# Optimization experiments

Measured on AMD Instinct MI355X. Metric: run time of the kernel, lower is better.

## Reference

```python
import jax, jax.numpy as jnp
import numpy as np

HEAD_DIM = 64
GRID = 4
DS = 4
EPS = 1e-6


def conv1x1(x, w, b):
    # x: (B,C,H,W), w: (O,C), b: (O,)
    return jnp.einsum('bchw,oc->bohw', x, w) + b[None, :, None, None]


def setup_inputs() -> dict:
    key = jax.random.key(0)
    ks = jax.random.split(key, 12)
    B, N, C = 16, 4096, 256
    s = 0.02
    return {
        'x': jax.random.normal(ks[0], (B, N, C), dtype=jnp.float32),
        'w_qkv': s * jax.random.normal(ks[1], (3 * C, C), dtype=jnp.float32),
        'b_qkv': jnp.zeros((3 * C,), dtype=jnp.float32),
        'w_q': s * jax.random.normal(ks[2], (C, C), dtype=jnp.float32),
        'b_q': jnp.zeros((C,), dtype=jnp.float32),
        'w_kv': s * jax.random.normal(ks[3], (2 * C, C), dtype=jnp.float32),
        'b_kv': jnp.zeros((2 * C,), dtype=jnp.float32),
        'w_proj': s * jax.random.normal(ks[4], (C, C), dtype=jnp.float32),
        'b_proj': jnp.zeros((C,), dtype=jnp.float32),
        'gn_w': jnp.ones((C,), dtype=jnp.float32),
        'gn_b': jnp.zeros((C,), dtype=jnp.float32),
    }


def reference(x, w_qkv, b_qkv, w_q, b_q, w_kv, b_kv, w_proj, b_proj, gn_w, gn_b):
    B, N, C = x.shape
    H = W = int(np.sqrt(N))
    hd = HEAD_DIM
    nh = C // hd
    gs = GRID
    scale = hd ** -0.5

    xi = x.transpose(0, 2, 1).reshape(B, C, H, W)
    qkv = conv1x1(xi, w_qkv, b_qkv)  # (B,3C,H,W)

    # ---- grid-window attention (gs x gs windows) ----
    gh, gw = H // gs, W // gs
    qkv = qkv.reshape(B, 3, nh, hd, gh, gs, gw, gs)
    qkv = qkv.transpose(1, 0, 2, 4, 6, 5, 7, 3).reshape(3, -1, gs * gs, hd)
    q, k, v = qkv[0], qkv[1], qkv[2]  # (B*nh*gh*gw, gs*gs, hd)
    attn = jax.nn.softmax(jnp.einsum('wqd,wkd->wqk', q, k) * scale, axis=-1)
    grid_x = jnp.einsum('wqk,wkd->wqd', attn, v)
    grid_x = grid_x.reshape(B, nh, gh, gw, gs, gs, hd)
    grid_x = grid_x.transpose(0, 1, 6, 2, 4, 3, 5).reshape(B, C, H, W)

    # channels_first LayerNorm(x + grid_x)
    z = xi + grid_x
    u = z.mean(1, keepdims=True)
    s2 = ((z - u) ** 2).mean(1, keepdims=True)
    grid_x = gn_w[None, :, None, None] * ((z - u) / jnp.sqrt(s2 + EPS)) + gn_b[None, :, None, None]

    # ---- pooled global attention ----
    qg = conv1x1(grid_x, w_q, b_q).reshape(B, nh, hd, N).transpose(0, 1, 3, 2)  # (B,nh,N,hd)
    pooled = grid_x.reshape(B, C, H // DS, DS, W // DS, DS).mean(axis=(3, 5))
    kv = conv1x1(pooled, w_kv, b_kv).reshape(B, 2, nh, hd, -1).transpose(1, 0, 2, 4, 3)
    k, v = kv[0], kv[1]  # (B,nh,Np,hd)
    attn = jax.nn.softmax(jnp.einsum('bhqd,bhkd->bhqk', qg, k) * scale, axis=-1)
    global_x = jnp.einsum('bhqk,bhkd->bhqd', attn, v)
    global_x = global_x.transpose(0, 1, 3, 2).reshape(B, C, H, W) + grid_x

    out = conv1x1(global_x, w_proj, b_proj)
    return out.reshape(B, C, N).transpose(0, 2, 1)
```

## Files before the change

### kernel.cpp

```cpp
#include <hip/hip_runtime.h>
#include <cstddef>

#define SCALE 0.125f
#define LN_EPS 1e-6f

typedef __attribute__((ext_vector_type(8))) short bf16x8;
typedef __attribute__((ext_vector_type(4))) float f32x4;

__device__ __forceinline__ unsigned short f2bf(float f) {
    unsigned u = __float_as_uint(f);
    return (unsigned short)((u + 0x7FFFu + ((u >> 16) & 1u)) >> 16);
}
__device__ __forceinline__ unsigned pack2(float a, float b) {
    return (unsigned)f2bf(a) | ((unsigned)f2bf(b) << 16);
}
__device__ __forceinline__ float bflo(unsigned v) { return __uint_as_float(v << 16); }
__device__ __forceinline__ float bfhi(unsigned v) { return __uint_as_float(v & 0xFFFF0000u); }
__device__ __forceinline__ float bf2f(short s) { return __uint_as_float(((unsigned)(unsigned short)s) << 16); }

#define GLOAD16(gp, lp) __builtin_amdgcn_global_load_lds( \
    (const __attribute__((address_space(1))) void*)(gp),  \
    (__attribute__((address_space(3))) void*)(lp), 16, 0, 0)

__global__ __launch_bounds__(256) void k_castw(
    const float* __restrict__ wqkv, const float* __restrict__ wq,
    const float* __restrict__ wkv, const float* __restrict__ wproj,
    short* __restrict__ wb)
{
    const int blk = blockIdx.x;
    const float* src; size_t so, doff;
    if (blk < 96)       { src = wqkv;  so = (size_t)blk * 2048;         doff = 0; }
    else if (blk < 128) { src = wq;    so = (size_t)(blk - 96) * 2048;  doff = 196608; }
    else if (blk < 192) { src = wkv;   so = (size_t)(blk - 128) * 2048; doff = 262144; }
    else                { src = wproj; so = (size_t)(blk - 192) * 2048; doff = 393216; }
    const size_t idx = so + (size_t)threadIdx.x * 8;
    const float4 f0 = *(const float4*)(src + idx);
    const float4 f1 = *(const float4*)(src + idx + 4);
    uint4 o;
    o.x = pack2(f0.x, f0.y); o.y = pack2(f0.z, f0.w);
    o.z = pack2(f1.x, f1.y); o.w = pack2(f1.z, f1.w);
    *(uint4*)(wb + doff + idx) = o;
}

__global__ __launch_bounds__(256) void k_castx(
    const float* __restrict__ x, short* __restrict__ xb)
{
    const size_t i = ((size_t)blockIdx.x * 256 + threadIdx.x) * 8;
    const float4 f0 = *(const float4*)(x + i);
    const float4 f1 = *(const float4*)(x + i + 4);
    uint4 o;
    o.x = pack2(f0.x, f0.y); o.y = pack2(f0.z, f0.w);
    o.z = pack2(f1.x, f1.y); o.w = pack2(f1.z, f1.w);
    *(uint4*)(xb + i) = o;
}

template<int OUTMODE>
__global__ __launch_bounds__(256, 2) void k_gemm(
    const short* __restrict__ Asrc, const short* __restrict__ Bw,
    const float* __restrict__ bias, void* __restrict__ Cdst,
    short* __restrict__ Vdst, int ldc, int nbn)
{
    __shared__ short As[2][128 * 64];
    __shared__ short Bs[2][128 * 64];

    const int tid = threadIdx.x;
    const int q8 = gridDim.x >> 3;
    const int bid = (blockIdx.x & 7) * q8 + (blockIdx.x >> 3);
    const int bm = bid / nbn, bn = bid % nbn;
    const size_t m0 = (size_t)bm * 128, n0 = (size_t)bn * 128;
    const int wid = tid >> 6, lane = tid & 63;
    const int wr = wid >> 1, wc = wid & 1;
    const int g = lane >> 4, r = lane & 15;
    const int rowc = lane >> 3, gran = lane & 7;

    f32x4 acc[4][4];
    #pragma unroll
    for (int mi = 0; mi < 4; ++mi)
        #pragma unroll
        for (int nj = 0; nj < 4; ++nj) acc[mi][nj] = (f32x4)0.f;

    auto STAGE = [&](int kt, int bufi) {
        const int k0 = kt * 64;
        #pragma unroll
        for (int i = 0; i < 4; ++i) {
            const int rbase = wid * 32 + i * 8;
            const int row = rbase + rowc;
            const int sg = gran ^ (row & 7);
            GLOAD16(Asrc + (m0 + row) * 256 + k0 + sg * 8, &As[bufi][rbase * 64]);
            GLOAD16(Bw   + (n0 + row) * 256 + k0 + sg * 8, &Bs[bufi][rbase * 64]);
        }
    };

    auto COMPUTE = [&](int bufi) {
        #pragma unroll
        for (int ks = 0; ks < 2; ++ks) {
            const int ke = ks * 32 + g * 8;
            bf16x8 a[4], b[4];
            #pragma unroll
            for (int mi = 0; mi < 4; ++mi) {
                const int row = wr * 64 + mi * 16 + r;
                a[mi] = *(const bf16x8*)&As[bufi][row * 64 + (ke ^ ((row & 7) << 3))];
            }
            #pragma unroll
            for (int nj = 0; nj < 4; ++nj) {
                const int row = wc * 64 + nj * 16 + r;
                b[nj] = *(const bf16x8*)&Bs[bufi][row * 64 + (ke ^ ((row & 7) << 3))];
            }
            #pragma unroll
            for (int mi = 0; mi < 4; ++mi)
                #pragma unroll
                for (int nj = 0; nj < 4; ++nj)
                    acc[mi][nj] = __builtin_amdgcn_mfma_f32_16x16x32_bf16(
                        a[mi], b[nj], acc[mi][nj], 0, 0, 0);
        }
    };

    STAGE(0, 0);
    __syncthreads();
    #pragma unroll
    for (int kt = 0; kt < 4; ++kt) {
        const int cur = kt & 1;
        if (kt < 3) STAGE(kt + 1, cur ^ 1);
        COMPUTE(cur);
        __syncthreads();
    }

    #pragma unroll
    for (int nj = 0; nj < 4; ++nj) {
        const size_t col = n0 + wc * 64 + nj * 16 + r;
        const float bv = bias[col];
        #pragma unroll
        for (int mi = 0; mi < 4; ++mi) {
            const size_t row = m0 + wr * 64 + mi * 16 + g * 4;
            #pragma unroll
            for (int e = 0; e < 4; ++e) {
                const float v = acc[mi][nj][e] + bv;
                const size_t rr = row + e;
                if (OUTMODE == 0) ((float*)Cdst)[rr * ldc + col] = v;
                else if (OUTMODE == 1) ((short*)Cdst)[rr * ldc + col] = (short)f2bf(v);
                else {
                    const int colk = (int)col - 256;
                    if (colk < 0) ((short*)Cdst)[rr * 256 + col] = (short)f2bf(v);
                    else {
                        const int hh = colk >> 6, dd = colk & 63;
                        Vdst[((((rr >> 8) * 4 + hh) * 64 + dd) << 8) + (rr & 255)] = (short)f2bf(v);
                    }
                }
            }
        }
    }
}

__global__ __launch_bounds__(256) void k_vtr(
    const short* __restrict__ qkvb, short* __restrict__ vwb)
{
    __shared__ short Vl[16][260];
    const int tid = threadIdx.x;
    const int blk = blockIdx.x;
    const int b = blk >> 8, win = blk & 255;
    const int ghi = win >> 4, gwi = win & 15;
    const size_t nb = (size_t)b * 4096;

    #pragma unroll
    for (int i = 0; i < 2; ++i) {
        const int c = i * 256 + tid;
        const int tok = c >> 5, ch = c & 31;
        const int n = (ghi * 4 + (tok >> 2)) * 64 + gwi * 4 + (tok & 3);
        const uint4 u = *(const uint4*)(qkvb + (nb + n) * 768 + 512 + ch * 8);
        short* dst = &Vl[tok][ch * 8];
        *(uint2*)dst = make_uint2(u.x, u.y);
        *(uint2*)(dst + 4) = make_uint2(u.z, u.w);
    }
    __syncthreads();

    unsigned w[8];
    #pragma unroll
    for (int k = 0; k < 8; ++k) {
        const unsigned lo = (unsigned)(unsigned short)Vl[2 * k][tid];
        const unsigned hi = (unsigned)(unsigned short)Vl[2 * k + 1][tid];
        w[k] = lo | (hi << 16);
    }
    short* dst = vwb + ((size_t)blk * 256 + tid) * 16;
    *(uint4*)dst = make_uint4(w[0], w[1], w[2], w[3]);
    *(uint4*)(dst + 8) = make_uint4(w[4], w[5], w[6], w[7]);
}

__global__ __launch_bounds__(256) void k_win3(
    const short* __restrict__ qkvb, const short* __restrict__ vwb,
    const short* __restrict__ xb, const float* __restrict__ gnw,
    const float* __restrict__ gnb, short* __restrict__ lnb,
    short* __restrict__ pooledb)
{
    __shared__ float zbuf[16][260];
    __shared__ short Pb[4][16][40];

    const int tid = threadIdx.x;
    const int blk = blockIdx.x;
    const int b = blk >> 8, win = blk & 255;
    const int ghi = win >> 4, gwi = win & 15;
    const size_t nb = (size_t)b * 4096;
    const int h = tid >> 6, lane = tid & 63;
    const int g = lane >> 4, l15 = lane & 15;

    const int n15 = (ghi * 4 + (l15 >> 2)) * 64 + gwi * 4 + (l15 & 3);
    const size_t qkrow = (nb + n15) * 768;
    const bf16x8 aq0 = *(const bf16x8*)(qkvb + qkrow + h * 64 + g * 8);
    const bf16x8 aq1 = *(const bf16x8*)(qkvb + qkrow + h * 64 + 32 + g * 8);
    const bf16x8 bk0 = *(const bf16x8*)(qkvb + qkrow + 256 + h * 64 + g * 8);
    const bf16x8 bk1 = *(const bf16x8*)(qkvb + qkrow + 256 + h * 64 + 32 + g * 8);

    f32x4 acc = (f32x4)0.f;
    acc = __builtin_amdgcn_mfma_f32_16x16x32_bf16(aq0, bk0, acc, 0, 0, 0);
    acc = __builtin_amdgcn_mfma_f32_16x16x32_bf16(aq1, bk1, acc, 0, 0, 0);

    float p[4];
    #pragma unroll
    for (int e = 0; e < 4; ++e) {
        const float s = acc[e] * SCALE;
        float mm = s;
        mm = fmaxf(mm, __shfl_xor(mm, 1)); mm = fmaxf(mm, __shfl_xor(mm, 2));
        mm = fmaxf(mm, __shfl_xor(mm, 4)); mm = fmaxf(mm, __shfl_xor(mm, 8));
        const float pe = __expf(s - mm);
        float rs = pe;
        rs += __shfl_xor(rs, 1); rs += __shfl_xor(rs, 2);
        rs += __shfl_xor(rs, 4); rs += __shfl_xor(rs, 8);
        p[e] = pe / rs;
    }
    #pragma unroll
    for (int e = 0; e < 4; ++e) {
        Pb[h][g * 4 + e][l15] = (short)f2bf(p[e]);
        Pb[h][g * 4 + e][16 + l15] = 0;
    }
    __syncthreads();

    const bf16x8 ap = *(const bf16x8*)&Pb[h][l15][g * 8];
    f32x4 oc[4];
    #pragma unroll
    for (int nt = 0; nt < 4; ++nt) oc[nt] = (f32x4)0.f;
    const short* vbase = vwb + ((((size_t)b * 256 + win) * 4 + h) << 10);
    #pragma unroll
    for (int nt = 0; nt < 4; ++nt) {
        const bf16x8 bv = *(const bf16x8*)(vbase + (nt * 16 + l15) * 16 + g * 8);
        oc[nt] = __builtin_amdgcn_mfma_f32_16x16x32_bf16(ap, bv, oc[nt], 0, 0, 0);
    }
    #pragma unroll
    for (int e = 0; e < 4; ++e)
        #pragma unroll
        for (int nt = 0; nt < 4; ++nt)
            zbuf[g * 4 + e][h * 64 + nt * 16 + l15] = oc[nt][e];
    __syncthreads();

    {
        const float4 gw = ((const float4*)gnw)[lane];
        const float4 gb = ((const float4*)gnb)[lane];
        #pragma unroll
        for (int i = 0; i < 4; ++i) {
            const int t = h * 4 + i;
            const int n = (ghi * 4 + (t >> 2)) * 64 + gwi * 4 + (t & 3);
            float4 zv = *(const float4*)&zbuf[t][lane * 4];
            const short4 xv = *(const short4*)(xb + (nb + n) * 256 + lane * 4);
            zv.x += bf2f(xv.x); zv.y += bf2f(xv.y);
            zv.z += bf2f(xv.z); zv.w += bf2f(xv.w);
            float ssum = zv.x + zv.y + zv.z + zv.w;
            for (int off = 1; off < 64; off <<= 1) ssum += __shfl_xor(ssum, off);
            const float u = ssum * (1.f / 256.f);
            const float dx = zv.x - u, dy = zv.y - u, dz = zv.z - u, dw = zv.w - u;
            float vsum = dx * dx + dy * dy + dz * dz + dw * dw;
            for (int off = 1; off < 64; off <<= 1) vsum += __shfl_xor(vsum, off);
            const float rinv = rsqrtf(vsum * (1.f / 256.f) + LN_EPS);
            float4 y;
            y.x = gw.x * dx * rinv + gb.x;
            y.y = gw.y * dy * rinv + gb.y;
            y.z = gw.z * dz * rinv + gb.z;
            y.w = gw.w * dw * rinv + gb.w;
            *(float4*)&zbuf[t][lane * 4] = y;
            short4 sv;
            sv.x = (short)f2bf(y.x); sv.y = (short)f2bf(y.y);
            sv.z = (short)f2bf(y.z); sv.w = (short)f2bf(y.w);
            *(short4*)(lnb + (nb + n) * 256 + lane * 4) = sv;
        }
    }
    __syncthreads();

    {
        float ps = 0.f;
        #pragma unroll
        for (int t = 0; t < 16; ++t) ps += zbuf[t][tid];
        pooledb[((size_t)b * 256 + win) * 256 + tid] = (short)f2bf(ps * (1.f / 16.f));
    }
}

#define CP 280
__global__ __launch_bounds__(512, 1) void k_glb(
    const short* __restrict__ qgb, const short* __restrict__ kb,
    const short* __restrict__ vtb, const short* __restrict__ lnb,
    short* __restrict__ gxb)
{
    __shared__ short Ks[256 * 64];
    __shared__ short Vt[64 * 256];
    __shared__ short Pl[8][16 * CP];

    const int tid = threadIdx.x;
    const int bid = (blockIdx.x & 7) * 256 + (blockIdx.x >> 3);
    const int bh = bid >> 5, qt = bid & 31;
    const int b = bh >> 2, h = bh & 3;
    const int q0 = qt * 128;
    const size_t nb = (size_t)b * 4096;

    #pragma unroll
    for (int i = 0; i < 4; ++i) {
        const int c = i * 512 + tid;
        const int p = c >> 3, d8 = (c & 7) * 8;
        const uint4 u = *(const uint4*)(kb + ((size_t)(b * 256 + p)) * 256 + h * 64 + d8);
        *(uint4*)&Ks[p * 64 + (d8 ^ ((p & 7) << 3))] = u;
    }
    const short* vsrc = vtb + (size_t)bh * 16384;
    #pragma unroll
    for (int i = 0; i < 4; ++i) {
        const int c = i * 512 + tid;
        const int d = c >> 5, k8 = (c & 31) * 8;
        const uint4 u = *(const uint4*)(vsrc + d * 256 + k8);
        *(uint4*)&Vt[d * 256 + (k8 ^ ((d & 7) << 3))] = u;
    }
    __syncthreads();

    const int w = tid >> 6, lane = tid & 63;
    const int g = lane >> 4, l15 = lane & 15;

    bf16x8 aq[2];
    {
        const int n = q0 + w * 16 + l15;
        const short* qp = qgb + (nb + n) * 256 + h * 64 + g * 8;
        aq[0] = *(const bf16x8*)qp;
        aq[1] = *(const bf16x8*)(qp + 32);
    }

    f32x4 acc[16];
    #pragma unroll
    for (int nt = 0; nt < 16; ++nt) acc[nt] = (f32x4)0.f;

    #pragma unroll
    for (int nt = 0; nt < 16; ++nt) {
        const int key = nt * 16 + l15;
        const int sw = (key & 7) << 3;
        const bf16x8 bk0 = *(const bf16x8*)&Ks[key * 64 + ((g * 8) ^ sw)];
        const bf16x8 bk1 = *(const bf16x8*)&Ks[key * 64 + ((g * 8 + 32) ^ sw)];
        acc[nt] = __builtin_amdgcn_mfma_f32_16x16x32_bf16(aq[0], bk0, acc[nt], 0, 0, 0);
        acc[nt] = __builtin_amdgcn_mfma_f32_16x16x32_bf16(aq[1], bk1, acc[nt], 0, 0, 0);
    }

    float rs[4];
    short* Pw = &Pl[w][0];
    #pragma unroll
    for (int e = 0; e < 4; ++e) {
        const int prow = (g * 4 + e) * CP;
        float rsum = 0.f;
        #pragma unroll
        for (int nt = 0; nt < 16; ++nt) {
            const float p = __expf(acc[nt][e] * SCALE);
            rsum += p;
            Pw[prow + nt * 16 + l15] = (short)f2bf(p);
        }
        rs[e] = rsum;
    }
    #pragma unroll
    for (int e = 0; e < 4; ++e) {
        float v = rs[e];
        v += __shfl_xor(v, 1); v += __shfl_xor(v, 2);
        v += __shfl_xor(v, 4); v += __shfl_xor(v, 8);
        rs[e] = v;
    }

    f32x4 oc[4];
    #pragma unroll
    for (int nt = 0; nt < 4; ++nt) oc[nt] = (f32x4)0.f;

    #pragma unroll
    for (int ks = 0; ks < 8; ++ks) {
        const int kc = ks * 32 + g * 8;
        const bf16x8 a0 = *(const bf16x8*)&Pw[l15 * CP + kc];
        #pragma unroll
        for (int nt = 0; nt < 4; ++nt) {
            const int d = nt * 16 + l15;
            const bf16x8 bv = *(const bf16x8*)&Vt[d * 256 + (kc ^ ((d & 7) << 3))];
            oc[nt] = __builtin_amdgcn_mfma_f32_16x16x32_bf16(a0, bv, oc[nt], 0, 0, 0);
        }
    }

    #pragma unroll
    for (int e = 0; e < 4; ++e) {
        const float inv = 1.f / rs[e];
        const int n = q0 + w * 16 + g * 4 + e;
        const size_t base = (nb + n) * 256 + h * 64;
        #pragma unroll
        for (int nt = 0; nt < 4; ++nt) {
            const int d = nt * 16 + l15;
            gxb[base + d] = (short)f2bf(oc[nt][e] * inv + bf2f(lnb[base + d]));
        }
    }
}

extern "C" void kernel_launch(void* const* d_in, const int* in_sizes, int n_in,
                              void* d_out, int out_size, void* d_ws, size_t ws_size,
                              hipStream_t stream)
{
    (void)in_sizes; (void)n_in; (void)out_size; (void)ws_size;
    const float* x     = (const float*)d_in[0];
    const float* wqkv  = (const float*)d_in[1];
    const float* bqkv  = (const float*)d_in[2];
    const float* wq    = (const float*)d_in[3];
    const float* bq    = (const float*)d_in[4];
    const float* wkv   = (const float*)d_in[5];
    const float* bkv   = (const float*)d_in[6];
    const float* wproj = (const float*)d_in[7];
    const float* bproj = (const float*)d_in[8];
    const float* gnw   = (const float*)d_in[9];
    const float* gnb   = (const float*)d_in[10];
    float* out = (float*)d_out;

    char* wsb = (char*)d_ws;
    short* wb      = (short*)(wsb + 0);
    short* qkvb    = (short*)(wsb + 1048576);
    short* lnb     = (short*)(wsb + 101711872);
    short* qgb     = (short*)(wsb + 135266304);
    short* kb      = (short*)(wsb + 168820736);
    short* vtb     = (short*)(wsb + 170917888);
    short* pooledb = (short*)(wsb + 173015040);
    short* gxb     = (short*)(wsb + 175112192);
    short* vwb     = gxb;
    short* xb      = (short*)(wsb + 208666624);

    k_castw<<<dim3(224),  dim3(256), 0, stream>>>(wqkv, wq, wkv, wproj, wb);
    k_castx<<<dim3(8192), dim3(256), 0, stream>>>(x, xb);
    k_gemm<1><<<dim3(3072), dim3(256), 0, stream>>>(xb, wb, bqkv, qkvb, nullptr, 768, 6);
    k_vtr<<<dim3(4096), dim3(256), 0, stream>>>(qkvb, vwb);
    k_win3<<<dim3(4096), dim3(256), 0, stream>>>(qkvb, vwb, xb, gnw, gnb, lnb, pooledb);
    k_gemm<1><<<dim3(1024), dim3(256), 0, stream>>>(lnb, wb + 196608, bq, qgb, nullptr, 256, 2);
    k_gemm<2><<<dim3(128), dim3(256), 0, stream>>>(pooledb, wb + 262144, bkv, kb, vtb, 512, 4);
    k_glb<<<dim3(2048), dim3(512), 0, stream>>>(qgb, kb, vtb, lnb, gxb);
    k_gemm<0><<<dim3(1024), dim3(256), 0, stream>>>(gxb, wb + 393216, bproj, out, nullptr, 256, 2);
}
```

Before: 212.5 us.

## Chunk global attention keys in two halves and stage GEMM bf16 output via LDS

```diff
diff --git a/kernel.cpp b/kernel.cpp
--- a/kernel.cpp
+++ b/kernel.cpp
@@ -60,8 +60,9 @@
     const float* __restrict__ bias, void* __restrict__ Cdst,
     short* __restrict__ Vdst, int ldc, int nbn)
 {
-    __shared__ short As[2][128 * 64];
-    __shared__ short Bs[2][128 * 64];
+    __shared__ short Sh[32768];
+    short* const As0 = Sh;
+    short* const Bs0 = Sh + 16384;
 
     const int tid = threadIdx.x;
     const int q8 = gridDim.x >> 3;
@@ -86,12 +87,14 @@
             const int rbase = wid * 32 + i * 8;
             const int row = rbase + rowc;
             const int sg = gran ^ (row & 7);
-            GLOAD16(Asrc + (m0 + row) * 256 + k0 + sg * 8, &As[bufi][rbase * 64]);
-            GLOAD16(Bw   + (n0 + row) * 256 + k0 + sg * 8, &Bs[bufi][rbase * 64]);
+            GLOAD16(Asrc + (m0 + row) * 256 + k0 + sg * 8, As0 + bufi * 8192 + rbase * 64);
+            GLOAD16(Bw   + (n0 + row) * 256 + k0 + sg * 8, Bs0 + bufi * 8192 + rbase * 64);
         }
     };
 
     auto COMPUTE = [&](int bufi) {
+        const short* A = As0 + bufi * 8192;
+        const short* B = Bs0 + bufi * 8192;
         #pragma unroll
         for (int ks = 0; ks < 2; ++ks) {
             const int ke = ks * 32 + g * 8;
@@ -99,12 +102,12 @@
             #pragma unroll
             for (int mi = 0; mi < 4; ++mi) {
                 const int row = wr * 64 + mi * 16 + r;
-                a[mi] = *(const bf16x8*)&As[bufi][row * 64 + (ke ^ ((row & 7) << 3))];
+                a[mi] = *(const bf16x8*)&A[row * 64 + (ke ^ ((row & 7) << 3))];
             }
             #pragma unroll
             for (int nj = 0; nj < 4; ++nj) {
                 const int row = wc * 64 + nj * 16 + r;
-                b[nj] = *(const bf16x8*)&Bs[bufi][row * 64 + (ke ^ ((row & 7) << 3))];
+                b[nj] = *(const bf16x8*)&B[row * 64 + (ke ^ ((row & 7) << 3))];
             }
             #pragma unroll
             for (int mi = 0; mi < 4; ++mi)
@@ -125,25 +128,49 @@
         __syncthreads();
     }
 
-    #pragma unroll
-    for (int nj = 0; nj < 4; ++nj) {
-        const size_t col = n0 + wc * 64 + nj * 16 + r;
-        const float bv = bias[col];
-        #pragma unroll
-        for (int mi = 0; mi < 4; ++mi) {
-            const size_t row = m0 + wr * 64 + mi * 16 + g * 4;
-            #pragma unroll
-            for (int e = 0; e < 4; ++e) {
-                const float v = acc[mi][nj][e] + bv;
-                const size_t rr = row + e;
-                if (OUTMODE == 0) ((float*)Cdst)[rr * ldc + col] = v;
-                else if (OUTMODE == 1) ((short*)Cdst)[rr * ldc + col] = (short)f2bf(v);
-                else {
-                    const int colk = (int)col - 256;
-                    if (colk < 0) ((short*)Cdst)[rr * 256 + col] = (short)f2bf(v);
+    if (OUTMODE == 1) {
+        short* const Cl = Sh;
+        #pragma unroll
+        for (int nj = 0; nj < 4; ++nj) {
+            const int col = wc * 64 + nj * 16 + r;
+            const float bv = bias[n0 + col];
+            #pragma unroll
+            for (int mi = 0; mi < 4; ++mi) {
+                const int row = wr * 64 + mi * 16 + g * 4;
+                #pragma unroll
+                for (int e = 0; e < 4; ++e)
+                    Cl[(row + e) * 132 + col] = (short)f2bf(acc[mi][nj][e] + bv);
+            }
+        }
+        __syncthreads();
+        short* C = (short*)Cdst;
+        #pragma unroll
+        for (int j = 0; j < 8; ++j) {
+            const int row = j * 16 + (tid >> 4);
+            const int c8 = (tid & 15) * 8;
+            const uint4 v = *(const uint4*)&Cl[row * 132 + c8];
+            *(uint4*)(C + (m0 + row) * ldc + n0 + c8) = v;
+        }
+    } else {
+        #pragma unroll
+        for (int nj = 0; nj < 4; ++nj) {
+            const size_t col = n0 + wc * 64 + nj * 16 + r;
+            const float bv = bias[col];
+            #pragma unroll
+            for (int mi = 0; mi < 4; ++mi) {
+                const size_t row = m0 + wr * 64 + mi * 16 + g * 4;
+                #pragma unroll
+                for (int e = 0; e < 4; ++e) {
+                    const float v = acc[mi][nj][e] + bv;
+                    const size_t rr = row + e;
+                    if (OUTMODE == 0) ((float*)Cdst)[rr * ldc + col] = v;
                     else {
-                        const int hh = colk >> 6, dd = colk & 63;
-                        Vdst[((((rr >> 8) * 4 + hh) * 64 + dd) << 8) + (rr & 255)] = (short)f2bf(v);
+                        const int colk = (int)col - 256;
+                        if (colk < 0) ((short*)Cdst)[rr * 256 + col] = (short)f2bf(v);
+                        else {
+                            const int hh = colk >> 6, dd = colk & 63;
+                            Vdst[((((rr >> 8) * 4 + hh) * 64 + dd) << 8) + (rr & 255)] = (short)f2bf(v);
+                        }
                     }
                 }
             }
@@ -290,14 +317,14 @@
     }
 }
 
-#define CP 280
-__global__ __launch_bounds__(512, 1) void k_glb(
+#define CP 136
+__global__ __launch_bounds__(512, 4) void k_glb(
     const short* __restrict__ qgb, const short* __restrict__ kb,
     const short* __restrict__ vtb, const short* __restrict__ lnb,
     short* __restrict__ gxb)
 {
-    __shared__ short Ks[256 * 64];
-    __shared__ short Vt[64 * 256];
+    __shared__ short Ks[128 * 64];
+    __shared__ short Vt[64 * 128];
     __shared__ short Pl[8][16 * CP];
 
     const int tid = threadIdx.x;
@@ -307,23 +334,6 @@
     const int q0 = qt * 128;
     const size_t nb = (size_t)b * 4096;
 
-    #pragma unroll
-    for (int i = 0; i < 4; ++i) {
-        const int c = i * 512 + tid;
-        const int p = c >> 3, d8 = (c & 7) * 8;
-        const uint4 u = *(const uint4*)(kb + ((size_t)(b * 256 + p)) * 256 + h * 64 + d8);
-        *(uint4*)&Ks[p * 64 + (d8 ^ ((p & 7) << 3))] = u;
-    }
-    const short* vsrc = vtb + (size_t)bh * 16384;
-    #pragma unroll
-    for (int i = 0; i < 4; ++i) {
-        const int c = i * 512 + tid;
-        const int d = c >> 5, k8 = (c & 31) * 8;
-        const uint4 u = *(const uint4*)(vsrc + d * 256 + k8);
-        *(uint4*)&Vt[d * 256 + (k8 ^ ((d & 7) << 3))] = u;
-    }
-    __syncthreads();
-
     const int w = tid >> 6, lane = tid & 63;
     const int g = lane >> 4, l15 = lane & 15;
 
@@ -335,56 +345,78 @@
         aq[1] = *(const bf16x8*)(qp + 32);
     }
 
-    f32x4 acc[16];
-    #pragma unroll
-    for (int nt = 0; nt < 16; ++nt) acc[nt] = (f32x4)0.f;
-
-    #pragma unroll
-    for (int nt = 0; nt < 16; ++nt) {
-        const int key = nt * 16 + l15;
-        const int sw = (key & 7) << 3;
-        const bf16x8 bk0 = *(const bf16x8*)&Ks[key * 64 + ((g * 8) ^ sw)];
-        const bf16x8 bk1 = *(const bf16x8*)&Ks[key * 64 + ((g * 8 + 32) ^ sw)];
-        acc[nt] = __builtin_amdgcn_mfma_f32_16x16x32_bf16(aq[0], bk0, acc[nt], 0, 0, 0);
-        acc[nt] = __builtin_amdgcn_mfma_f32_16x16x32_bf16(aq[1], bk1, acc[nt], 0, 0, 0);
-    }
-
-    float rs[4];
+    f32x4 oc[4];
+    #pragma unroll
+    for (int nt = 0; nt < 4; ++nt) oc[nt] = (f32x4)0.f;
+    float rs[4] = {0.f, 0.f, 0.f, 0.f};
+
+    const short* ksrc = kb + ((size_t)b * 256) * 256 + h * 64;
+    const short* vsrc = vtb + (size_t)bh * 16384;
     short* Pw = &Pl[w][0];
-    #pragma unroll
-    for (int e = 0; e < 4; ++e) {
-        const int prow = (g * 4 + e) * CP;
-        float rsum = 0.f;
-        #pragma unroll
-        for (int nt = 0; nt < 16; ++nt) {
-            const float p = __expf(acc[nt][e] * SCALE);
-            rsum += p;
-            Pw[prow + nt * 16 + l15] = (short)f2bf(p);
-        }
-        rs[e] = rsum;
-    }
+
+    for (int c = 0; c < 2; ++c) {
+        if (c) __syncthreads();
+        #pragma unroll
+        for (int i = 0; i < 2; ++i) {
+            const int cc = i * 512 + tid;
+            const int p = cc >> 3, d8 = (cc & 7) * 8;
+            const uint4 u = *(const uint4*)(ksrc + (size_t)(c * 128 + p) * 256 + d8);
+            *(uint4*)&Ks[p * 64 + (d8 ^ ((p & 7) << 3))] = u;
+        }
+        #pragma unroll
+        for (int i = 0; i < 2; ++i) {
+            const int cc = i * 512 + tid;
+            const int d = cc >> 4, k8 = (cc & 15) * 8;
+            const uint4 u = *(const uint4*)(vsrc + d * 256 + c * 128 + k8);
+            *(uint4*)&Vt[d * 128 + (k8 ^ ((d & 7) << 3))] = u;
+        }
+        __syncthreads();
+
+        f32x4 acc[8];
+        #pragma unroll
+        for (int nt = 0; nt < 8; ++nt) acc[nt] = (f32x4)0.f;
+        #pragma unroll
+        for (int nt = 0; nt < 8; ++nt) {
+            const int key = nt * 16 + l15;
+            const int sw = (key & 7) << 3;
+            const bf16x8 bk0 = *(const bf16x8*)&Ks[key * 64 + ((g * 8) ^ sw)];
+            const bf16x8 bk1 = *(const bf16x8*)&Ks[key * 64 + ((g * 8 + 32) ^ sw)];
+            acc[nt] = __builtin_amdgcn_mfma_f32_16x16x32_bf16(aq[0], bk0, acc[nt], 0, 0, 0);
+            acc[nt] = __builtin_amdgcn_mfma_f32_16x16x32_bf16(aq[1], bk1, acc[nt], 0, 0, 0);
+        }
+
+        #pragma unroll
+        for (int e = 0; e < 4; ++e) {
+            const int prow = (g * 4 + e) * CP;
+            float rsum = 0.f;
+            #pragma unroll
+            for (int nt = 0; nt < 8; ++nt) {
+                const float p = __expf(acc[nt][e] * SCALE);
+                rsum += p;
+                Pw[prow + nt * 16 + l15] = (short)f2bf(p);
+            }
+            rs[e] += rsum;
+        }
+
+        #pragma unroll
+        for (int ks = 0; ks < 4; ++ks) {
+            const int kc = ks * 32 + g * 8;
+            const bf16x8 a0 = *(const bf16x8*)&Pw[l15 * CP + kc];
+            #pragma unroll
+            for (int nt = 0; nt < 4; ++nt) {
+                const int d = nt * 16 + l15;
+                const bf16x8 bv = *(const bf16x8*)&Vt[d * 128 + (kc ^ ((d & 7) << 3))];
+                oc[nt] = __builtin_amdgcn_mfma_f32_16x16x32_bf16(a0, bv, oc[nt], 0, 0, 0);
+            }
+        }
+    }
+
     #pragma unroll
     for (int e = 0; e < 4; ++e) {
         float v = rs[e];
         v += __shfl_xor(v, 1); v += __shfl_xor(v, 2);
         v += __shfl_xor(v, 4); v += __shfl_xor(v, 8);
         rs[e] = v;
-    }
-
-    f32x4 oc[4];
-    #pragma unroll
-    for (int nt = 0; nt < 4; ++nt) oc[nt] = (f32x4)0.f;
-
-    #pragma unroll
-    for (int ks = 0; ks < 8; ++ks) {
-        const int kc = ks * 32 + g * 8;
-        const bf16x8 a0 = *(const bf16x8*)&Pw[l15 * CP + kc];
-        #pragma unroll
-        for (int nt = 0; nt < 4; ++nt) {
-            const int d = nt * 16 + l15;
-            const bf16x8 bv = *(const bf16x8*)&Vt[d * 256 + (kc ^ ((d & 7) << 3))];
-            oc[nt] = __builtin_amdgcn_mfma_f32_16x16x32_bf16(a0, bv, oc[nt], 0, 0, 0);
-        }
     }
 
     #pragma unroll
```

After: 198.5 us. 1.07x faster.
